# Performance work log

Measured on AMD Instinct MI355X. Metric: run time of the kernel, lower is better.

## Reference

```python
import jax, jax.numpy as jnp
import numpy as np

N = 2_000_000  # hits
D = 4          # track-parameter dim
P = 50_000     # number of particle ids (0 = noise)


def setup_inputs() -> dict:
    key = jax.random.key(0)
    k1, k2, k3, k4, k5 = jax.random.split(key, 5)
    # beta in (0, 1) open interval so arctanh stays finite
    beta = jax.random.uniform(k1, (N,), jnp.float32, 0.01, 0.99)
    pred = jax.random.normal(k2, (N, D), jnp.float32)
    track_params = jax.random.normal(k3, (N, D), jnp.float32)
    particle_id = jax.random.randint(k4, (N,), 0, P)
    reconstructable = jax.random.randint(k5, (N,), 0, 2)
    return {
        "beta": beta,
        "pred": pred,
        "particle_id": particle_id,
        "track_params": track_params,
        "reconstructable": reconstructable,
    }


def reference(beta, pred, particle_id, track_params, reconstructable):
    # mask = reconstructable > 0; instead of gathering a dynamic subset,
    # route masked-out hits (and pid==0 noise) to segment 0, which is dropped.
    valid = reconstructable > 0
    seg = jnp.where(valid, particle_id, 0)

    # per-hit squared-error summed over parameter dim (mse_loss reduction='none' then sum(dim=1))
    mse = jnp.sum((pred - track_params) ** 2, axis=1)  # [N]
    xi = jnp.arctanh(beta) ** 2                         # [N]

    # segmented replacement of the dense N x P pid_masks broadcast:
    # terms_p = sum_i mse_i * xi_i * [pid_i == p], xi_p_norm_p = sum_i xi_i * [pid_i == p]
    num = jax.ops.segment_sum(mse * xi, seg, num_segments=P)  # [P]
    den = jax.ops.segment_sum(xi, seg, num_segments=P)        # [P]

    # mean over real particle ids 1..P-1 (segment 0 holds noise + masked hits)
    return jnp.mean(num[1:] / den[1:])
```

## Files before the change

### kernel.cpp

```cpp
#include <hip/hip_runtime.h>
#include <stdint.h>

#define P_IDS   50000
#define NBUCK   32
#define BUCK_W  1563
#define HPT     8
#define BLK_HITS (256 * HPT)
#define M_PER   64
#define SUBB    16


__global__ void __launch_bounds__(256)
phaseA_bucket(const float* __restrict__ beta,
              const float4* __restrict__ pred,
              const int* __restrict__ pid_arr,
              const float4* __restrict__ track,
              const int* __restrict__ recon,
              int* __restrict__ cnt_arr,
              uint2* __restrict__ recs,
              float* __restrict__ out,
              int n, int nblk) {
    __shared__ uint2 stage[NBUCK * M_PER];
    __shared__ int cursor[NBUCK];
    const int t = threadIdx.x;
    if (t < NBUCK) cursor[t] = 0;
    if (blockIdx.x == 0 && t == 0) *out = 0.0f;
    __syncthreads();

    const int B = blockIdx.x * BLK_HITS;

    int    p_[HPT], r_[HPT];
    float  b_[HPT];
    float4 pr_[HPT], tp_[HPT];
    #pragma unroll
    for (int h = 0; h < HPT; ++h) {
        int i = B + h * 256 + t;
        if (i < n) {
            p_[h]  = pid_arr[i];
            r_[h]  = recon[i];
            b_[h]  = beta[i];
            pr_[h] = pred[i];
            tp_[h] = track[i];
        } else {
            p_[h] = 0; r_[h] = 0; b_[h] = 0.5f;
            pr_[h] = make_float4(0.f,0.f,0.f,0.f);
            tp_[h] = make_float4(0.f,0.f,0.f,0.f);
        }
    }

    #pragma unroll
    for (int h = 0; h < HPT; ++h) {
        int p = p_[h], r = r_[h];
        if (r > 0 && p > 0) {
            float4 pr = pr_[h], tp = tp_[h];
            float dx = pr.x - tp.x, dy = pr.y - tp.y;
            float dz = pr.z - tp.z, dw = pr.w - tp.w;
            float mse = dx*dx + dy*dy + dz*dz + dw*dw;
            float at = 0.5f * logf((1.0f + b_[h]) / (1.0f - b_[h]));
            float xi = at * at;
            int bb = p / BUCK_W;
            int pl = p - bb * BUCK_W;
            int rank = atomicAdd(&cursor[bb], 1);
            if (rank < M_PER) {
                uint2 rr;
                rr.x = (__float_as_uint(xi) & 0xFFFFF800u) | (uint32_t)pl;
                rr.y = __float_as_uint(mse * xi);
                stage[bb * M_PER + rank] = rr;
            }
        }
    }
    __syncthreads();

    const uint4* src = (const uint4*)stage;
    uint4* dst = (uint4*)(recs + (size_t)blockIdx.x * (NBUCK * M_PER));
    #pragma unroll
    for (int k = 0; k < 4; ++k)
        dst[t + k * 256] = src[t + k * 256];

    if (t < NBUCK)
        cnt_arr[blockIdx.x * NBUCK + t] = min(cursor[t], M_PER);
}

__global__ void __launch_bounds__(256)
phaseB_bin(const int* __restrict__ cnt_arr,
           const uint2* __restrict__ recs,
           float2* __restrict__ partials,
           int nblk) {
    __shared__ float2 hist[BUCK_W];
    int part = blockIdx.x / SUBB;
    int sub  = blockIdx.x % SUBB;

    for (int j = threadIdx.x; j < BUCK_W; j += 256)
        hist[j] = make_float2(0.0f, 0.0f);
    __syncthreads();

    int lane  = threadIdx.x & 63;
    int wid   = threadIdx.x >> 6;
    int wslot = sub * 4 + wid;
    const int nslots = SUBB * 4;

    for (int b = wslot; b < nblk; b += nslots) {
        int cnt = cnt_arr[b * NBUCK + part];
        const uint2* r = recs + ((size_t)b * NBUCK + part) * M_PER;
        for (int idx = lane; idx < cnt; idx += 64) {
            uint2 rr = r[idx];
            int   pl  = rr.x & 0x7FFu;
            float xi  = __uint_as_float(rr.x & 0xFFFFF800u);
            float num = __uint_as_float(rr.y);
            atomicAdd(&hist[pl].x, num);
            atomicAdd(&hist[pl].y, xi);
        }
    }
    __syncthreads();

    float2* dst = partials + (size_t)blockIdx.x * BUCK_W;
    for (int j = threadIdx.x; j < BUCK_W; j += 256)
        dst[j] = hist[j];
}

__global__ void __launch_bounds__(256)
phaseC_mean(const float2* __restrict__ partials,
            float* __restrict__ out) {
    double local = 0.0;
    int stride = gridDim.x * blockDim.x;
    for (int p = 1 + blockIdx.x * blockDim.x + threadIdx.x; p < P_IDS; p += stride) {
        int part = p / BUCK_W;
        int loc  = p % BUCK_W;
        const float2* base = partials + ((size_t)part * SUBB) * BUCK_W + loc;
        float num = 0.0f, den = 0.0f;
        #pragma unroll
        for (int s = 0; s < SUBB; ++s) {
            float2 v = base[(size_t)s * BUCK_W];
            num += v.x;
            den += v.y;
        }
        local += (double)(num / den);
    }

    for (int off = 32; off > 0; off >>= 1)
        local += __shfl_down(local, off, 64);

    __shared__ double wave_sums[4];
    int lane = threadIdx.x & 63;
    int wid  = threadIdx.x >> 6;
    if (lane == 0) wave_sums[wid] = local;
    __syncthreads();

    if (threadIdx.x == 0) {
        double s = wave_sums[0] + wave_sums[1] + wave_sums[2] + wave_sums[3];
        atomicAdd(out, (float)(s / (double)(P_IDS - 1)));
    }
}

__global__ void __launch_bounds__(256)
scatter_fallback(const float* __restrict__ beta,
                 const float4* __restrict__ pred,
                 const int* __restrict__ pid,
                 const float4* __restrict__ track,
                 const int* __restrict__ recon,
                 float2* __restrict__ bins, int n) {
    int i = blockIdx.x * blockDim.x + threadIdx.x;
    if (i >= n) return;
    int p = pid[i];
    int r = recon[i];
    if (r <= 0 || p <= 0) return;
    float  b  = beta[i];
    float4 pr = pred[i];
    float4 tp = track[i];
    float dx = pr.x - tp.x, dy = pr.y - tp.y, dz = pr.z - tp.z, dw = pr.w - tp.w;
    float mse = dx*dx + dy*dy + dz*dz + dw*dw;
    float at = 0.5f * logf((1.0f + b) / (1.0f - b));
    float xi = at * at;
    atomicAdd(&bins[p].x, mse * xi);
    atomicAdd(&bins[p].y, xi);
}

__global__ void __launch_bounds__(256)
reduce_fallback(const float2* __restrict__ bins, float* __restrict__ out) {
    double local = 0.0;
    int stride = gridDim.x * blockDim.x;
    for (int p = 1 + blockIdx.x * blockDim.x + threadIdx.x; p < P_IDS; p += stride) {
        float2 v = bins[p];
        local += (double)(v.x / v.y);
    }
    for (int off = 32; off > 0; off >>= 1)
        local += __shfl_down(local, off, 64);
    __shared__ double wave_sums[4];
    int lane = threadIdx.x & 63;
    int wid  = threadIdx.x >> 6;
    if (lane == 0) wave_sums[wid] = local;
    __syncthreads();
    if (threadIdx.x == 0) {
        double s = wave_sums[0] + wave_sums[1] + wave_sums[2] + wave_sums[3];
        atomicAdd(out, (float)(s / (double)(P_IDS - 1)));
    }
}

extern "C" void kernel_launch(void* const* d_in, const int* in_sizes, int n_in,
                              void* d_out, int out_size, void* d_ws, size_t ws_size,
                              hipStream_t stream) {
    const float*  beta  = (const float*)d_in[0];
    const float4* pred  = (const float4*)d_in[1];
    const int*    pid   = (const int*)d_in[2];
    const float4* track = (const float4*)d_in[3];
    const int*    recon = (const int*)d_in[4];
    float* out = (float*)d_out;
    int n = in_sizes[0];

    int nblk = (n + BLK_HITS - 1) / BLK_HITS;

    size_t recs_bytes = sizeof(uint2) * (size_t)nblk * NBUCK * M_PER;
    size_t recs_pad   = (recs_bytes + 255) & ~(size_t)255;
    size_t cnt_bytes  = sizeof(int) * (size_t)nblk * NBUCK;
    size_t cnt_pad    = (cnt_bytes + 255) & ~(size_t)255;
    size_t part_bytes = sizeof(float2) * (size_t)NBUCK * SUBB * BUCK_W;
    size_t needed = recs_pad + cnt_pad + part_bytes;

    if (ws_size >= needed) {
        uint2*  recs     = (uint2*)d_ws;
        int*    cnt_arr  = (int*)((char*)d_ws + recs_pad);
        float2* partials = (float2*)((char*)d_ws + recs_pad + cnt_pad);

        phaseA_bucket<<<nblk, 256, 0, stream>>>(beta, pred, pid, track, recon,
                                                cnt_arr, recs, out, n, nblk);
        phaseB_bin<<<NBUCK * SUBB, 256, 0, stream>>>(cnt_arr, recs, partials, nblk);
        phaseC_mean<<<196, 256, 0, stream>>>(partials, out);
    } else {
        float2* bins = (float2*)d_ws;
        hipMemsetAsync(bins, 0, P_IDS * sizeof(float2), stream);
        hipMemsetAsync(d_out, 0, sizeof(float), stream);
        int grid = (n + 255) / 256;
        scatter_fallback<<<grid, 256, 0, stream>>>(beta, pred, pid, track, recon,
                                                   bins, n);
        reduce_fallback<<<196, 256, 0, stream>>>(bins, out);
    }
}
```

Measured before the change: 132.9 us.

## Compact bucket records, split waves across two blocks, fuse final mean into binning

Phase A now stores only the filled records of each bucket contiguously, using a per-block prefix sum, and packs offset and count into one word, so less workspace is written and read. Phase B splits each wave into two half-waves that work on different source blocks, which uses more lanes when buckets are short. The last block to finish each partition, tracked by an atomic done counter, performs the final mean reduction, which removes the separate phaseC kernel launch. This relies on a threadfence and an acquire-release atomic for correctness, and the count packing assumes offsets fit in 16 bits.

```diff
diff --git a/kernel.cpp b/kernel.cpp
--- a/kernel.cpp
+++ b/kernel.cpp
@@ -18,13 +18,18 @@
               const int* __restrict__ recon,
               int* __restrict__ cnt_arr,
               uint2* __restrict__ recs,
+              int* __restrict__ done,
               float* __restrict__ out,
               int n, int nblk) {
     __shared__ uint2 stage[NBUCK * M_PER];
     __shared__ int cursor[NBUCK];
+    __shared__ int prefx[NBUCK];
     const int t = threadIdx.x;
     if (t < NBUCK) cursor[t] = 0;
-    if (blockIdx.x == 0 && t == 0) *out = 0.0f;
+    if (blockIdx.x == 0) {
+        if (t < NBUCK) done[t] = 0;
+        if (t == NBUCK) *out = 0.0f;
+    }
     __syncthreads();
 
     const int B = blockIdx.x * BLK_HITS;
@@ -71,22 +76,42 @@
     }
     __syncthreads();
 
-    const uint4* src = (const uint4*)stage;
-    uint4* dst = (uint4*)(recs + (size_t)blockIdx.x * (NBUCK * M_PER));
+    if (t < 64) {
+        int c = (t < NBUCK) ? min(cursor[t], M_PER) : 0;
+        int x = c;
+        #pragma unroll
+        for (int d = 1; d < NBUCK; d <<= 1) {
+            int y = __shfl_up(x, d, 64);
+            if (t >= d) x += y;
+        }
+        if (t < NBUCK) {
+            int excl = x - c;
+            prefx[t] = excl;
+            cnt_arr[blockIdx.x * NBUCK + t] = (excl << 16) | c;
+        }
+    }
+    __syncthreads();
+
+    uint2* dst = recs + (size_t)blockIdx.x * (NBUCK * M_PER);
     #pragma unroll
-    for (int k = 0; k < 4; ++k)
-        dst[t + k * 256] = src[t + k * 256];
-
-    if (t < NBUCK)
-        cnt_arr[blockIdx.x * NBUCK + t] = min(cursor[t], M_PER);
+    for (int k = 0; k < 8; ++k) {
+        int slot = t + k * 256;
+        int bb = slot >> 6, rank = slot & 63;
+        if (rank < min(cursor[bb], M_PER))
+            dst[prefx[bb] + rank] = stage[slot];
+    }
 }
 
 __global__ void __launch_bounds__(256)
 phaseB_bin(const int* __restrict__ cnt_arr,
            const uint2* __restrict__ recs,
            float2* __restrict__ partials,
+           int* __restrict__ done,
+           float* __restrict__ out,
            int nblk) {
     __shared__ float2 hist[BUCK_W];
+    __shared__ double wsum[4];
+    __shared__ int s_last;
     int part = blockIdx.x / SUBB;
     int sub  = blockIdx.x % SUBB;
 
@@ -95,20 +120,26 @@
     __syncthreads();
 
     int lane  = threadIdx.x & 63;
+    int half  = lane >> 5;
+    int hlane = lane & 31;
     int wid   = threadIdx.x >> 6;
     int wslot = sub * 4 + wid;
     const int nslots = SUBB * 4;
 
-    for (int b = wslot; b < nblk; b += nslots) {
-        int cnt = cnt_arr[b * NBUCK + part];
-        const uint2* r = recs + ((size_t)b * NBUCK + part) * M_PER;
-        for (int idx = lane; idx < cnt; idx += 64) {
-            uint2 rr = r[idx];
-            int   pl  = rr.x & 0x7FFu;
-            float xi  = __uint_as_float(rr.x & 0xFFFFF800u);
-            float num = __uint_as_float(rr.y);
-            atomicAdd(&hist[pl].x, num);
-            atomicAdd(&hist[pl].y, xi);
+    for (int bp = wslot * 2; bp < nblk; bp += nslots * 2) {
+        int b = bp + half;
+        if (b < nblk) {
+            int pc  = cnt_arr[b * NBUCK + part];
+            int off = pc >> 16, cnt = pc & 0xFFFF;
+            const uint2* r = recs + (size_t)b * (NBUCK * M_PER) + off;
+            for (int idx = hlane; idx < cnt; idx += 32) {
+                uint2 rr = r[idx];
+                int   pl  = rr.x & 0x7FFu;
+                float xi  = __uint_as_float(rr.x & 0xFFFFF800u);
+                float num = __uint_as_float(rr.y);
+                atomicAdd(&hist[pl].x, num);
+                atomicAdd(&hist[pl].y, xi);
+            }
         }
     }
     __syncthreads();
@@ -116,38 +147,37 @@
     float2* dst = partials + (size_t)blockIdx.x * BUCK_W;
     for (int j = threadIdx.x; j < BUCK_W; j += 256)
         dst[j] = hist[j];
-}
-
-__global__ void __launch_bounds__(256)
-phaseC_mean(const float2* __restrict__ partials,
-            float* __restrict__ out) {
+
+    __threadfence();
+    __syncthreads();
+    if (threadIdx.x == 0) {
+        int prev = __hip_atomic_fetch_add(&done[part], 1, __ATOMIC_ACQ_REL,
+                                          __HIP_MEMORY_SCOPE_AGENT);
+        s_last = (prev == SUBB - 1);
+    }
+    __syncthreads();
+    if (!s_last) return;
+
     double local = 0.0;
-    int stride = gridDim.x * blockDim.x;
-    for (int p = 1 + blockIdx.x * blockDim.x + threadIdx.x; p < P_IDS; p += stride) {
-        int part = p / BUCK_W;
-        int loc  = p % BUCK_W;
-        const float2* base = partials + ((size_t)part * SUBB) * BUCK_W + loc;
+    const float2* pb = partials + (size_t)part * SUBB * BUCK_W;
+    for (int j = threadIdx.x; j < BUCK_W; j += 256) {
+        int pg = part * BUCK_W + j;
         float num = 0.0f, den = 0.0f;
         #pragma unroll
         for (int s = 0; s < SUBB; ++s) {
-            float2 v = base[(size_t)s * BUCK_W];
+            float2 v = pb[(size_t)s * BUCK_W + j];
             num += v.x;
             den += v.y;
         }
-        local += (double)(num / den);
-    }
-
+        if (pg >= 1 && pg < P_IDS)
+            local += (double)(num / den);
+    }
     for (int off = 32; off > 0; off >>= 1)
         local += __shfl_down(local, off, 64);
-
-    __shared__ double wave_sums[4];
-    int lane = threadIdx.x & 63;
-    int wid  = threadIdx.x >> 6;
-    if (lane == 0) wave_sums[wid] = local;
-    __syncthreads();
-
+    if ((threadIdx.x & 63) == 0) wsum[threadIdx.x >> 6] = local;
+    __syncthreads();
     if (threadIdx.x == 0) {
-        double s = wave_sums[0] + wave_sums[1] + wave_sums[2] + wave_sums[3];
+        double s = wsum[0] + wsum[1] + wsum[2] + wsum[3];
         atomicAdd(out, (float)(s / (double)(P_IDS - 1)));
     }
 }
@@ -214,17 +244,20 @@
     size_t cnt_bytes  = sizeof(int) * (size_t)nblk * NBUCK;
     size_t cnt_pad    = (cnt_bytes + 255) & ~(size_t)255;
     size_t part_bytes = sizeof(float2) * (size_t)NBUCK * SUBB * BUCK_W;
-    size_t needed = recs_pad + cnt_pad + part_bytes;
+    size_t part_pad   = (part_bytes + 255) & ~(size_t)255;
+    size_t done_bytes = sizeof(int) * NBUCK;
+    size_t needed = recs_pad + cnt_pad + part_pad + done_bytes;
 
     if (ws_size >= needed) {
         uint2*  recs     = (uint2*)d_ws;
         int*    cnt_arr  = (int*)((char*)d_ws + recs_pad);
         float2* partials = (float2*)((char*)d_ws + recs_pad + cnt_pad);
+        int*    done     = (int*)((char*)d_ws + recs_pad + cnt_pad + part_pad);
 
         phaseA_bucket<<<nblk, 256, 0, stream>>>(beta, pred, pid, track, recon,
-                                                cnt_arr, recs, out, n, nblk);
-        phaseB_bin<<<NBUCK * SUBB, 256, 0, stream>>>(cnt_arr, recs, partials, nblk);
-        phaseC_mean<<<196, 256, 0, stream>>>(partials, out);
+                                                cnt_arr, recs, done, out, n, nblk);
+        phaseB_bin<<<NBUCK * SUBB, 256, 0, stream>>>(cnt_arr, recs, partials,
+                                                     done, out, nblk);
     } else {
         float2* bins = (float2*)d_ws;
         hipMemsetAsync(bins, 0, P_IDS * sizeof(float2), stream);
```

New measurement: 190.1 us. 1.43x slower.

## Compact per-block bucket records and split waves into half-wave readers

Applied to the files above, without the earlier changes.

Phase A now runs a wave-level prefix scan over the bucket counts and writes only the filled records, contiguously, instead of the full padded 64-slot staging area. Each count word packs the offset and the count. Phase B has each half-wave handle a different block, so two blocks are processed per wave, which suits the roughly 16-record buckets. This cuts global write and read traffic and wasted lanes, at the cost of an extra barrier, a scan and scattered writes.

```diff
diff --git a/kernel.cpp b/kernel.cpp
--- a/kernel.cpp
+++ b/kernel.cpp
@@ -22,6 +22,7 @@
               int n, int nblk) {
     __shared__ uint2 stage[NBUCK * M_PER];
     __shared__ int cursor[NBUCK];
+    __shared__ int prefx[NBUCK];
     const int t = threadIdx.x;
     if (t < NBUCK) cursor[t] = 0;
     if (blockIdx.x == 0 && t == 0) *out = 0.0f;
@@ -71,14 +72,30 @@
     }
     __syncthreads();
 
-    const uint4* src = (const uint4*)stage;
-    uint4* dst = (uint4*)(recs + (size_t)blockIdx.x * (NBUCK * M_PER));
+    if (t < 64) {
+        int c = (t < NBUCK) ? min(cursor[t], M_PER) : 0;
+        int x = c;
+        #pragma unroll
+        for (int d = 1; d < NBUCK; d <<= 1) {
+            int y = __shfl_up(x, d, 64);
+            if (t >= d) x += y;
+        }
+        if (t < NBUCK) {
+            int excl = x - c;
+            prefx[t] = excl;
+            cnt_arr[blockIdx.x * NBUCK + t] = (excl << 16) | c;
+        }
+    }
+    __syncthreads();
+
+    uint2* dst = recs + (size_t)blockIdx.x * (NBUCK * M_PER);
     #pragma unroll
-    for (int k = 0; k < 4; ++k)
-        dst[t + k * 256] = src[t + k * 256];
-
-    if (t < NBUCK)
-        cnt_arr[blockIdx.x * NBUCK + t] = min(cursor[t], M_PER);
+    for (int k = 0; k < 8; ++k) {
+        int slot = t + k * 256;
+        int bb = slot >> 6, rank = slot & 63;
+        if (rank < min(cursor[bb], M_PER))
+            dst[prefx[bb] + rank] = stage[slot];
+    }
 }
 
 __global__ void __launch_bounds__(256)
@@ -95,20 +112,26 @@
     __syncthreads();
 
     int lane  = threadIdx.x & 63;
+    int half  = lane >> 5;
+    int hlane = lane & 31;
     int wid   = threadIdx.x >> 6;
     int wslot = sub * 4 + wid;
     const int nslots = SUBB * 4;
 
-    for (int b = wslot; b < nblk; b += nslots) {
-        int cnt = cnt_arr[b * NBUCK + part];
-        const uint2* r = recs + ((size_t)b * NBUCK + part) * M_PER;
-        for (int idx = lane; idx < cnt; idx += 64) {
-            uint2 rr = r[idx];
-            int   pl  = rr.x & 0x7FFu;
-            float xi  = __uint_as_float(rr.x & 0xFFFFF800u);
-            float num = __uint_as_float(rr.y);
-            atomicAdd(&hist[pl].x, num);
-            atomicAdd(&hist[pl].y, xi);
+    for (int bp = wslot * 2; bp < nblk; bp += nslots * 2) {
+        int b = bp + half;
+        if (b < nblk) {
+            int pc  = cnt_arr[b * NBUCK + part];
+            int off = pc >> 16, cnt = pc & 0xFFFF;
+            const uint2* r = recs + (size_t)b * (NBUCK * M_PER) + off;
+            for (int idx = hlane; idx < cnt; idx += 32) {
+                uint2 rr = r[idx];
+                int   pl  = rr.x & 0x7FFu;
+                float xi  = __uint_as_float(rr.x & 0xFFFFF800u);
+                float num = __uint_as_float(rr.y);
+                atomicAdd(&hist[pl].x, num);
+                atomicAdd(&hist[pl].y, xi);
+            }
         }
     }
     __syncthreads();
```

Measured after the change: 130.9 us, median of 2. Within noise of the previous version (-1.5%).
